# Kernel tuning notes

Hardware: AMD Instinct MI355X
Metric: run time of the kernel (lower is better)

The kernel has to match this reference:

```python
import jax, jax.numpy as jnp
import numpy as np

E = 8        # n_routed_experts
K = 4        # num_experts_per_tok
T = 1024     # tokens
H = 1024     # hidden_size
I = 1408     # moe_intermediate_size


def setup_inputs() -> dict:
    key = jax.random.key(0)
    ks = jax.random.split(key, 6)
    hidden_states = jax.random.normal(ks[0], (T, H), jnp.float32)
    rw = jax.random.uniform(ks[1], (T, K), jnp.float32)
    router_weights = rw / jnp.sum(rw, axis=-1, keepdims=True)  # normalized top-k router weights
    selected_experts = jax.random.randint(ks[2], (T, K), 0, E, jnp.int32)
    gate_w = jax.random.normal(ks[3], (E, H, I), jnp.float32) * (H ** -0.5)  # lecun_normal-ish
    up_w = jax.random.normal(ks[4], (E, H, I), jnp.float32) * (H ** -0.5)
    down_w = jax.random.normal(ks[5], (E, I, H), jnp.float32) * (I ** -0.5)
    return {
        'hidden_states': hidden_states,
        'router_weights': router_weights,
        'gate_w': gate_w,
        'up_w': up_w,
        'down_w': down_w,
        'selected_experts': selected_experts,
    }


def _grouped_matmul(x, w, seg):
    # x: [m, k] tokens sorted by expert; w: [E, k, n]; seg: [m] expert id per row.
    # Grouped GEMM expressed as E masked GEMMs (fixed small loop over experts);
    # a custom kernel would do true variable-group-size grouped GEMM.
    out = jnp.zeros((x.shape[0], w.shape[-1]), x.dtype)
    for e in range(w.shape[0]):
        out = out + jnp.where((seg == e)[:, None], x, jnp.zeros((), x.dtype)) @ w[e]
    return out


def reference(hidden_states, router_weights, gate_w, up_w, down_w, selected_experts):
    t, k = selected_experts.shape
    flat = selected_experts.ravel()                       # [t*k]
    hs = jnp.repeat(hidden_states, k, axis=0)             # [t*k, H]
    sort_idx = jnp.argsort(flat)                          # dispatch: sort tokens by expert
    seg = flat[sort_idx]
    xs = hs[sort_idx]
    gate = _grouped_matmul(xs, gate_w, seg)               # [t*k, I]
    up = _grouped_matmul(xs, up_w, seg)                   # [t*k, I]
    h = jax.nn.silu(gate) * up                            # fused SwiGLU
    down = _grouped_matmul(h, down_w, seg)                # [t*k, H]
    unsort = jnp.argsort(sort_idx)                        # scatter back to token order
    out = down[unsort].reshape(t, k, -1)
    return jnp.sum(out * router_weights[..., None], axis=1)  # weighted combine [t, H]
```

## Files before the change

kernel.cpp:

```cpp
#include <hip/hip_runtime.h>
#include <hip/hip_bf16.h>
#include <cstdint>
#include <cstddef>

#define NE 8
#define NT 1024
#define NK 4
#define NH 1024
#define NI 1408
#define NA (NT * NK)
#define BM 128
#define MAXTILES 40
#define PADSLOTS 5120

typedef short short8 __attribute__((ext_vector_type(8)));
typedef float f32x4 __attribute__((ext_vector_type(4)));
typedef float f4v __attribute__((ext_vector_type(4)));
typedef unsigned short u16;

#define WS_HDR   0
#define WS_SORT  1024
#define WS_XBF   21504
#define WS_GT    2118656
#define WS_UT    25187328
#define WS_DT    48256000
#define WS_HB    71324672
#define WS_SLOT  (WS_HB + 4992 * NI * 2)
#define PART_PLANE (PADSLOTS * NH)

__device__ __forceinline__ u16 f2b(float f) {
  union { float f; uint32_t u; } c; c.f = f;
  uint32_t u = c.u;
  return (u16)((u + 0x7FFFu + ((u >> 16) & 1u)) >> 16);
}

__device__ __forceinline__ void llds16(const void* g, void* l) {
  __builtin_amdgcn_global_load_lds(
      (const __attribute__((address_space(1))) void*)g,
      (__attribute__((address_space(3))) void*)l, 16, 0, 0);
}

__device__ __forceinline__ void transcvt_stripe(const float* __restrict__ src,
                                                u16* __restrict__ dst,
                                                int K, int N, int k0, int n0,
                                                u16* smem, int tid) {
  u16 (*t2)[64][64] = (u16(*)[64][64])smem;
  int r = tid >> 4, c = tid & 15;
  f4v v[2][4];
#pragma unroll
  for (int t = 0; t < 2; ++t)
#pragma unroll
    for (int i = 0; i < 4; ++i)
      v[t][i] = __builtin_nontemporal_load(
          (const f4v*)&src[(size_t)(k0 + r + 16 * i) * N + n0 + t * 64 + c * 4]);
#pragma unroll
  for (int t = 0; t < 2; ++t)
#pragma unroll
    for (int i = 0; i < 4; ++i) {
      ushort4 o;
      o.x = f2b(v[t][i].x); o.y = f2b(v[t][i].y); o.z = f2b(v[t][i].z); o.w = f2b(v[t][i].w);
      int row = r + 16 * i;
      int sc = (c * 4) ^ (row & 56);
      *(ushort4*)&t2[t][row][sc] = o;
    }
  __syncthreads();
#pragma unroll
  for (int t = 0; t < 2; ++t)
#pragma unroll
    for (int i = 0; i < 2; ++i) {
      int idx = i * 256 + tid;
      int n = idx >> 3, kc = idx & 7;
      int cs = n ^ (kc * 8);
      u16 o[8];
#pragma unroll
      for (int j = 0; j < 8; ++j) o[j] = t2[t][kc * 8 + j][cs];
      *(short8*)&dst[(size_t)(n0 + t * 64 + n) * K + k0 + kc * 8] = *(const short8*)o;
    }
}

__global__ __launch_bounds__(256) void k1_prep(
    const float* __restrict__ gw, const float* __restrict__ uw, const float* __restrict__ dw,
    const float* __restrict__ hs, const int* __restrict__ sel,
    u16* __restrict__ gT, u16* __restrict__ uT, u16* __restrict__ dT, u16* __restrict__ xbf,
    int* __restrict__ hdr, int* __restrict__ sorted, int* __restrict__ slotOf) {
  int tid = threadIdx.x;
  int y = blockIdx.y;
  if (y == 24) {
    for (int i = blockIdx.x * 256 + tid; i * 4 < NT * NH; i += 176 * 256) {
      f4v v = __builtin_nontemporal_load((const f4v*)&hs[i * 4]);
      ushort4 o;
      o.x = f2b(v.x); o.y = f2b(v.y); o.z = f2b(v.z); o.w = f2b(v.w);
      *(ushort4*)&xbf[i * 4] = o;
    }
    return;
  }
  if (y == 25) {
    if (blockIdx.x != 0) return;
    __shared__ int cnt[NE], fill[NE], poff_s[NE + 1];
    if (tid < NE) { cnt[tid] = 0; fill[tid] = 0; }
    __syncthreads();
    for (int i = tid; i < NA; i += 256) atomicAdd(&cnt[sel[i]], 1);
    __syncthreads();
    if (tid == 0) {
      int off = 0, nt = 0;
      for (int e = 0; e < NE; ++e) {
        poff_s[e] = off;
        int tiles = (cnt[e] + BM - 1) / BM;
        for (int j = 0; j < tiles; ++j) { hdr[32 + nt] = e; hdr[80 + nt] = off + j * BM; ++nt; }
        off += tiles * BM;
      }
      poff_s[NE] = off;
      hdr[17] = nt;
      for (int e = 0; e < NE; ++e) hdr[e] = cnt[e];
      for (int e = 0; e <= NE; ++e) hdr[8 + e] = poff_s[e];
    }
    __syncthreads();
    for (int i = tid; i < PADSLOTS; i += 256) sorted[i] = -1;
    __syncthreads();
    for (int i = tid; i < NA; i += 256) {
      int e = sel[i];
      int p = atomicAdd(&fill[e], 1);
      int s = poff_s[e] + p;
      sorted[s] = i;
      slotOf[i] = s;
    }
    return;
  }
  __shared__ u16 smem[2 * 64 * 64];
  if (y < 16) {
    int tensor = y >> 3, e = y & 7;
    const float* src = ((tensor == 0) ? gw : uw) + (size_t)e * NH * NI;
    u16* dst = ((tensor == 0) ? gT : uT) + (size_t)e * NH * NI;
    int nb = blockIdx.x % 11, kb = blockIdx.x / 11;
    transcvt_stripe(src, dst, NH, NI, kb * 64, nb * 128, smem, tid);
  } else {
    int e = y - 16;
    const float* src = dw + (size_t)e * NI * NH;
    u16* dst = dT + (size_t)e * NI * NH;
    int nb = blockIdx.x % 8, kb = blockIdx.x / 8;
    transcvt_stripe(src, dst, NI, NH, kb * 64, nb * 128, smem, tid);
  }
}

__global__ __launch_bounds__(256, 2) void k2_gemm1(
    const u16* __restrict__ xbf, const u16* __restrict__ gT, const u16* __restrict__ uT,
    u16* __restrict__ hbuf, const int* __restrict__ hdr, const int* __restrict__ sorted) {
  __shared__ u16 smem[36864];
  int b = blockIdx.x;
  int tid = threadIdx.x;

  int job = (b & 7) * 55 + (b >> 3);
  int tile = job % 40;
  if (tile >= hdr[17]) return;
  int e = hdr[32 + tile];
  int slot0 = hdr[80 + tile];
  int n0 = (job / 40) * 128;

  const u16* aptr[2];
  const u16 *bgp[2], *bup[2];
#pragma unroll
  for (int s = 0; s < 2; ++s) {
    int idx = s * 256 + tid;
    int row = idx >> 2, c = idx & 3;
    int kc = c ^ (row & 3) ^ ((row >> 2) & 3);
    int as = sorted[slot0 + row];
    int trow = (as >= 0) ? (as >> 2) : 0;
    aptr[s] = xbf + (size_t)trow * NH + kc * 8;
    size_t o = ((size_t)e * NI + n0 + row) * NH + kc * 8;
    bgp[s] = gT + o; bup[s] = uT + o;
  }

  int lane = tid & 63, wave = tid >> 6;
  int wm = wave >> 1, wn = wave & 1;
  int l15 = lane & 15, quad = lane >> 4;
  int pos = ((quad ^ (l15 & 3) ^ ((l15 >> 2) & 3)) & 3) * 8;

  f32x4 accg[4][4] = {}; f32x4 accu[4][4] = {};

#define K2_STAGE(BUF, KT)                                                \
  {                                                                      \
    int ko_ = (KT) * 32;                                                 \
    u16* p_ = smem + (BUF) * 12288;                                      \
    llds16(aptr[0] + ko_, p_ + tid * 8);                                 \
    llds16(aptr[1] + ko_, p_ + (256 + tid) * 8);                         \
    llds16(bgp[0] + ko_, p_ + 4096 + tid * 8);                           \
    llds16(bgp[1] + ko_, p_ + 4096 + (256 + tid) * 8);                   \
    llds16(bup[0] + ko_, p_ + 8192 + tid * 8);                           \
    llds16(bup[1] + ko_, p_ + 8192 + (256 + tid) * 8);                   \
  }

  K2_STAGE(0, 0);
  K2_STAGE(1, 1);
  for (int kt = 0; kt < 32; ++kt) {
    if (kt == 31) { asm volatile("s_waitcnt vmcnt(0)" ::: "memory"); }
    else          { asm volatile("s_waitcnt vmcnt(6)" ::: "memory"); }
    __builtin_amdgcn_s_barrier();
    __builtin_amdgcn_sched_barrier(0);
    if (kt < 30) K2_STAGE((kt + 2) % 3, kt + 2);
    const u16* sA  = smem + (kt % 3) * 12288;
    const u16* sBg = sA + 4096;
    const u16* sBu = sA + 8192;
    short8 av[4], bg[4], bu[4];
#pragma unroll
    for (int mf = 0; mf < 4; ++mf)
      av[mf] = *(const short8*)&sA[(wm * 64 + mf * 16 + l15) * 32 + pos];
#pragma unroll
    for (int nf = 0; nf < 4; ++nf) {
      bg[nf] = *(const short8*)&sBg[(wn * 64 + nf * 16 + l15) * 32 + pos];
      bu[nf] = *(const short8*)&sBu[(wn * 64 + nf * 16 + l15) * 32 + pos];
    }
#pragma unroll
    for (int mf = 0; mf < 4; ++mf)
#pragma unroll
      for (int nf = 0; nf < 4; ++nf) {
        accg[mf][nf] = __builtin_amdgcn_mfma_f32_16x16x32_bf16(av[mf], bg[nf], accg[mf][nf], 0, 0, 0);
        accu[mf][nf] = __builtin_amdgcn_mfma_f32_16x16x32_bf16(av[mf], bu[nf], accu[mf][nf], 0, 0, 0);
      }
  }
#undef K2_STAGE

  for (int mf = 0; mf < 4; ++mf)
    for (int nf = 0; nf < 4; ++nf)
      for (int r = 0; r < 4; ++r) {
        int row = wm * 64 + mf * 16 + quad * 4 + r;
        int col = n0 + wn * 64 + nf * 16 + l15;
        float g2 = accg[mf][nf][r], u = accu[mf][nf][r];
        float hv = (g2 / (1.f + __expf(-g2))) * u;
        hbuf[(size_t)(slot0 + row) * NI + col] = f2b(hv);
      }
}

__global__ __launch_bounds__(256, 3) void k3_gemm2(
    const u16* __restrict__ hbuf, const u16* __restrict__ dT,
    const float* __restrict__ rw, float* __restrict__ part,
    const int* __restrict__ hdr, const int* __restrict__ sorted) {
  __shared__ u16 smem[24576];
  int b = blockIdx.x;
  int nsl = b & 7;
  int r = b >> 3;
  int tile = r % 40;
  int kh = r / 40;
  if (tile >= hdr[17]) return;
  int e = hdr[32 + tile];
  int slot0 = hdr[80 + tile];
  int n0 = nsl * 128;
  int tid = threadIdx.x;

  const u16 *ap[2], *bp[2];
#pragma unroll
  for (int s = 0; s < 2; ++s) {
    int idx = s * 256 + tid;
    int row = idx >> 2, c = idx & 3;
    int kc = c ^ (row & 3) ^ ((row >> 2) & 3);
    ap[s] = hbuf + (size_t)(slot0 + row) * NI + kc * 8;
    bp[s] = dT + ((size_t)e * NH + n0 + row) * NI + kc * 8;
  }

  int lane = tid & 63, wave = tid >> 6;
  int wm = wave >> 1, wn = wave & 1;
  int l15 = lane & 15, quad = lane >> 4;
  int pos = ((quad ^ (l15 & 3) ^ ((l15 >> 2) & 3)) & 3) * 8;

  f32x4 acc[4][4] = {};

#define K3_STAGE(BUF, KT)                                                \
  {                                                                      \
    int ko_ = (KT) * 32;                                                 \
    u16* p_ = smem + (BUF) * 8192;                                       \
    llds16(ap[0] + ko_, p_ + tid * 8);                                   \
    llds16(ap[1] + ko_, p_ + (256 + tid) * 8);                           \
    llds16(bp[0] + ko_, p_ + 4096 + tid * 8);                            \
    llds16(bp[1] + ko_, p_ + 4096 + (256 + tid) * 8);                    \
  }

  int kt0 = kh * 22;
  K3_STAGE(0, kt0);
  K3_STAGE(1, kt0 + 1);
  for (int kt = 0; kt < 22; ++kt) {
    if (kt == 21) { asm volatile("s_waitcnt vmcnt(0)" ::: "memory"); }
    else          { asm volatile("s_waitcnt vmcnt(4)" ::: "memory"); }
    __builtin_amdgcn_s_barrier();
    __builtin_amdgcn_sched_barrier(0);
    if (kt < 20) K3_STAGE((kt + 2) % 3, kt0 + kt + 2);
    const u16* sA = smem + (kt % 3) * 8192;
    const u16* sB = sA + 4096;
    short8 av[4], bv[4];
#pragma unroll
    for (int mf = 0; mf < 4; ++mf)
      av[mf] = *(const short8*)&sA[(wm * 64 + mf * 16 + l15) * 32 + pos];
#pragma unroll
    for (int nf = 0; nf < 4; ++nf)
      bv[nf] = *(const short8*)&sB[(wn * 64 + nf * 16 + l15) * 32 + pos];
#pragma unroll
    for (int mf = 0; mf < 4; ++mf)
#pragma unroll
      for (int nf = 0; nf < 4; ++nf)
        acc[mf][nf] = __builtin_amdgcn_mfma_f32_16x16x32_bf16(av[mf], bv[nf], acc[mf][nf], 0, 0, 0);
  }
#undef K3_STAGE

  float* plane = part + (size_t)kh * PART_PLANE;
  for (int mf = 0; mf < 4; ++mf) {
    int rowb = wm * 64 + mf * 16 + quad * 4;
    for (int rr = 0; rr < 4; ++rr) {
      int slot = slot0 + rowb + rr;
      int as = sorted[slot];
      if (as < 0) continue;
      float w = rw[as];
      float* prow = plane + (size_t)slot * NH + n0 + wn * 64;
      for (int nf = 0; nf < 4; ++nf)
        prow[nf * 16 + l15] = w * acc[mf][nf][rr];
    }
  }
}

__global__ __launch_bounds__(256) void k4_combine(
    const float* __restrict__ part, const int* __restrict__ slotOf,
    float* __restrict__ out) {
  int tid = threadIdx.x;
  int token = blockIdx.x * 2 + (tid >> 7);
  int col0 = (tid & 127) * 8;
  const int* sl = slotOf + token * 4;
  f4v a0 = {0.f, 0.f, 0.f, 0.f}, a1 = {0.f, 0.f, 0.f, 0.f};
#pragma unroll
  for (int k = 0; k < 4; ++k) {
    size_t ro = (size_t)sl[k] * NH + col0;
    const float* p0 = part + ro;
    const float* p1 = part + (size_t)PART_PLANE + ro;
    a0 += *(const f4v*)p0;
    a1 += *(const f4v*)(p0 + 4);
    a0 += *(const f4v*)p1;
    a1 += *(const f4v*)(p1 + 4);
  }
  float* o = out + (size_t)token * NH + col0;
  *(f4v*)o = a0;
  *(f4v*)(o + 4) = a1;
}

extern "C" void kernel_launch(void* const* d_in, const int* in_sizes, int n_in,
                              void* d_out, int out_size, void* d_ws, size_t ws_size,
                              hipStream_t stream) {
  const float* hs  = (const float*)d_in[0];
  const float* rw  = (const float*)d_in[1];
  const float* gw  = (const float*)d_in[2];
  const float* uw  = (const float*)d_in[3];
  const float* dw  = (const float*)d_in[4];
  const int*   sel = (const int*)d_in[5];
  float* out = (float*)d_out;

  char* ws = (char*)d_ws;
  int*  hdr    = (int*)(ws + WS_HDR);
  int*  sorted = (int*)(ws + WS_SORT);
  u16*  xbf    = (u16*)(ws + WS_XBF);
  u16*  gT     = (u16*)(ws + WS_GT);
  u16*  uT     = (u16*)(ws + WS_UT);
  u16*  dT     = (u16*)(ws + WS_DT);
  u16*  hb     = (u16*)(ws + WS_HB);
  float* part  = (float*)(ws + WS_GT);
  int*  slotOf = (int*)(ws + WS_SLOT);

  hipLaunchKernelGGL(k1_prep, dim3(176, 26), dim3(256), 0, stream,
                     gw, uw, dw, hs, sel, gT, uT, dT, xbf, hdr, sorted, slotOf);
  hipLaunchKernelGGL(k2_gemm1, dim3(440), dim3(256), 0, stream,
                     xbf, gT, uT, hb, hdr, sorted);
  hipLaunchKernelGGL(k3_gemm2, dim3(640), dim3(256), 0, stream,
                     hb, dT, rw, part, hdr, sorted);
  hipLaunchKernelGGL(k4_combine, dim3(512), dim3(256), 0, stream,
                     part, slotOf, out);
}
```

Measured before the change: 237.1 us.

## Double k-stripes per prep block and switch gemm1 to double-buffered LDS

The weight transpose-convert now has each block handle two 64-row k-stripes. It issues all 16 global loads up front, so memory latency is amortized across twice the work, and the prep grid is halved. The gate/up GEMM drops from a 3-stage to a 2-stage LDS ring, cutting shared memory from 72KB to 48KB and raising launch bounds to 3 blocks per CU for occupancy. In exchange, the GEMM now waits for all outstanding loads every k-step, which reduces prefetch depth and can expose load latency.

```diff
diff --git a/kernel.cpp b/kernel.cpp
--- a/kernel.cpp
+++ b/kernel.cpp
@@ -40,42 +40,50 @@
       (__attribute__((address_space(3))) void*)l, 16, 0, 0);
 }
 
-__device__ __forceinline__ void transcvt_stripe(const float* __restrict__ src,
-                                                u16* __restrict__ dst,
-                                                int K, int N, int k0, int n0,
-                                                u16* smem, int tid) {
+__device__ __forceinline__ void transcvt_pipe(const float* __restrict__ src,
+                                              u16* __restrict__ dst,
+                                              int K, int N, int k0a, int n0,
+                                              u16* smem, int tid) {
   u16 (*t2)[64][64] = (u16(*)[64][64])smem;
   int r = tid >> 4, c = tid & 15;
-  f4v v[2][4];
-#pragma unroll
-  for (int t = 0; t < 2; ++t)
-#pragma unroll
-    for (int i = 0; i < 4; ++i)
-      v[t][i] = __builtin_nontemporal_load(
-          (const f4v*)&src[(size_t)(k0 + r + 16 * i) * N + n0 + t * 64 + c * 4]);
-#pragma unroll
-  for (int t = 0; t < 2; ++t)
-#pragma unroll
-    for (int i = 0; i < 4; ++i) {
-      ushort4 o;
-      o.x = f2b(v[t][i].x); o.y = f2b(v[t][i].y); o.z = f2b(v[t][i].z); o.w = f2b(v[t][i].w);
-      int row = r + 16 * i;
-      int sc = (c * 4) ^ (row & 56);
-      *(ushort4*)&t2[t][row][sc] = o;
-    }
-  __syncthreads();
-#pragma unroll
-  for (int t = 0; t < 2; ++t)
-#pragma unroll
-    for (int i = 0; i < 2; ++i) {
-      int idx = i * 256 + tid;
-      int n = idx >> 3, kc = idx & 7;
-      int cs = n ^ (kc * 8);
-      u16 o[8];
-#pragma unroll
-      for (int j = 0; j < 8; ++j) o[j] = t2[t][kc * 8 + j][cs];
-      *(short8*)&dst[(size_t)(n0 + t * 64 + n) * K + k0 + kc * 8] = *(const short8*)o;
-    }
+  f4v v[2][2][4];
+#pragma unroll
+  for (int s2 = 0; s2 < 2; ++s2)
+#pragma unroll
+    for (int t = 0; t < 2; ++t)
+#pragma unroll
+      for (int i = 0; i < 4; ++i)
+        v[s2][t][i] = __builtin_nontemporal_load(
+            (const f4v*)&src[(size_t)(k0a + s2 * 64 + r + 16 * i) * N + n0 + t * 64 + c * 4]);
+#pragma unroll
+  for (int s2 = 0; s2 < 2; ++s2) {
+    int k0 = k0a + s2 * 64;
+    if (s2) __syncthreads();
+#pragma unroll
+    for (int t = 0; t < 2; ++t)
+#pragma unroll
+      for (int i = 0; i < 4; ++i) {
+        ushort4 o;
+        o.x = f2b(v[s2][t][i].x); o.y = f2b(v[s2][t][i].y);
+        o.z = f2b(v[s2][t][i].z); o.w = f2b(v[s2][t][i].w);
+        int row = r + 16 * i;
+        int sc = (c * 4) ^ (row & 56);
+        *(ushort4*)&t2[t][row][sc] = o;
+      }
+    __syncthreads();
+#pragma unroll
+    for (int t = 0; t < 2; ++t)
+#pragma unroll
+      for (int i = 0; i < 2; ++i) {
+        int idx = i * 256 + tid;
+        int n = idx >> 3, kc = idx & 7;
+        int cs = n ^ (kc * 8);
+        u16 o[8];
+#pragma unroll
+        for (int j = 0; j < 8; ++j) o[j] = t2[t][kc * 8 + j][cs];
+        *(short8*)&dst[(size_t)(n0 + t * 64 + n) * K + k0 + kc * 8] = *(const short8*)o;
+      }
+  }
 }
 
 __global__ __launch_bounds__(256) void k1_prep(
@@ -86,7 +94,7 @@
   int tid = threadIdx.x;
   int y = blockIdx.y;
   if (y == 24) {
-    for (int i = blockIdx.x * 256 + tid; i * 4 < NT * NH; i += 176 * 256) {
+    for (int i = blockIdx.x * 256 + tid; i * 4 < NT * NH; i += 88 * 256) {
       f4v v = __builtin_nontemporal_load((const f4v*)&hs[i * 4]);
       ushort4 o;
       o.x = f2b(v.x); o.y = f2b(v.y); o.z = f2b(v.z); o.w = f2b(v.w);
@@ -131,21 +139,21 @@
     int tensor = y >> 3, e = y & 7;
     const float* src = ((tensor == 0) ? gw : uw) + (size_t)e * NH * NI;
     u16* dst = ((tensor == 0) ? gT : uT) + (size_t)e * NH * NI;
-    int nb = blockIdx.x % 11, kb = blockIdx.x / 11;
-    transcvt_stripe(src, dst, NH, NI, kb * 64, nb * 128, smem, tid);
+    int nb = blockIdx.x % 11, kbp = blockIdx.x / 11;
+    transcvt_pipe(src, dst, NH, NI, kbp * 128, nb * 128, smem, tid);
   } else {
     int e = y - 16;
     const float* src = dw + (size_t)e * NI * NH;
     u16* dst = dT + (size_t)e * NI * NH;
-    int nb = blockIdx.x % 8, kb = blockIdx.x / 8;
-    transcvt_stripe(src, dst, NI, NH, kb * 64, nb * 128, smem, tid);
-  }
-}
-
-__global__ __launch_bounds__(256, 2) void k2_gemm1(
+    int nb = blockIdx.x % 8, kbp = blockIdx.x / 8;
+    transcvt_pipe(src, dst, NI, NH, kbp * 128, nb * 128, smem, tid);
+  }
+}
+
+__global__ __launch_bounds__(256, 3) void k2_gemm1(
     const u16* __restrict__ xbf, const u16* __restrict__ gT, const u16* __restrict__ uT,
     u16* __restrict__ hbuf, const int* __restrict__ hdr, const int* __restrict__ sorted) {
-  __shared__ u16 smem[36864];
+  __shared__ u16 smem[24576];
   int b = blockIdx.x;
   int tid = threadIdx.x;
 
@@ -190,14 +198,12 @@
   }
 
   K2_STAGE(0, 0);
-  K2_STAGE(1, 1);
   for (int kt = 0; kt < 32; ++kt) {
-    if (kt == 31) { asm volatile("s_waitcnt vmcnt(0)" ::: "memory"); }
-    else          { asm volatile("s_waitcnt vmcnt(6)" ::: "memory"); }
+    asm volatile("s_waitcnt vmcnt(0)" ::: "memory");
     __builtin_amdgcn_s_barrier();
     __builtin_amdgcn_sched_barrier(0);
-    if (kt < 30) K2_STAGE((kt + 2) % 3, kt + 2);
-    const u16* sA  = smem + (kt % 3) * 12288;
+    if (kt < 31) K2_STAGE((kt + 1) & 1, kt + 1);
+    const u16* sA  = smem + (kt & 1) * 12288;
     const u16* sBg = sA + 4096;
     const u16* sBu = sA + 8192;
     short8 av[4], bg[4], bu[4];
@@ -359,7 +365,7 @@
   float* part  = (float*)(ws + WS_GT);
   int*  slotOf = (int*)(ws + WS_SLOT);
 
-  hipLaunchKernelGGL(k1_prep, dim3(176, 26), dim3(256), 0, stream,
+  hipLaunchKernelGGL(k1_prep, dim3(88, 26), dim3(256), 0, stream,
                      gw, uw, dw, hs, sel, gT, uT, dT, xbf, hdr, sorted, slotOf);
   hipLaunchKernelGGL(k2_gemm1, dim3(440), dim3(256), 0, stream,
                      xbf, gT, uT, hb, hdr, sorted);
```

After: 267.1 us. +12.7%, slower.
